# Performance work log

Measured on AMD Instinct MI355X. Metric: run time of the kernel, lower is better.

## Reference

```python
import jax, jax.numpy as jnp
import numpy as np
from jax import lax

F8 = jnp.float8_e4m3fn


def setup_inputs() -> dict:
    key = jax.random.key(0)
    kx, kw = jax.random.split(key)
    x = jax.random.normal(kx, (2, 128, 4, 192, 320), dtype=jnp.float32)
    # matches reset_parameters: normal(0, 0.02) then cast to fp8
    weight = jax.random.normal(kw, (128, 128, 3, 3, 3), dtype=jnp.float32) * 0.02
    return {"x": x, "weight": weight}


def reference(x, weight):
    # fp8 e4m3 quantization round-trip (the torch module stores/consumes fp8),
    # compute/accumulate in fp32 as an fp8 conv kernel would.
    xq = x.astype(F8).astype(jnp.float32)
    wq = weight.astype(F8).astype(jnp.float32)
    # causal temporal padding: (kT-1, 0) = (2, 0); spatial 'same' padding (1,1)
    xp = jnp.pad(xq, ((0, 0), (0, 0), (2, 0), (1, 1), (1, 1)))
    out = lax.conv_general_dilated(
        xp, wq,
        window_strides=(1, 1, 1),
        padding='VALID',
        dimension_numbers=('NCDHW', 'OIDHW', 'NCDHW'),
    )  # (B, 128, 4, 192, 320)
    return out
```

## Files before the change

kernel.cpp:

```cpp
#include <hip/hip_runtime.h>
#include <hip/hip_fp8.h>


using f32x16 = __attribute__((ext_vector_type(16))) float;
using i32x8 = __attribute__((ext_vector_type(8))) int;
typedef long long i64;
struct alignas(16) L2v { i64 x, y; };

namespace {
constexpr int Cc = 128, Dd = 4, Hh = 192, Ww = 320;
constexpr int HP = 194, WP = 322;
constexpr int NTAP = 27;
constexpr size_t PLANE = (size_t)4 * WP * 32;
constexpr size_t XQ_BYTES = (size_t)2 * Dd * HP * PLANE;
constexpr int ZA = 8 * 2 * 2576;
constexpr int ZB = 8 * 192 * 32;
constexpr int GSTR = WP * 32;
constexpr int HB = 1056;
}

__global__ __launch_bounds__(256) void zero_pad_kernel(unsigned char* __restrict__ xq) {
  int i = blockIdx.x * 256 + threadIdx.x;
  if (i < ZA) {
    int bd = i / (2 * 2576);
    int r = i - bd * (2 * 2576);
    int hsel = r / 2576, seg = r - hsel * 2576;
    L2v z{0, 0};
    *(L2v*)(xq + ((size_t)bd * HP + (hsel ? 193 : 0)) * PLANE + (size_t)seg * 16) = z;
  } else if (i < ZA + ZB) {
    int j = i - ZA;
    int bd = j / (192 * 32);
    int r = j - bd * (192 * 32);
    int h = r / 32 + 1;
    int t = r & 31;
    int g = t >> 3, s2 = t & 7;
    int wsel = s2 >> 2, part = s2 & 3;
    *(i64*)(xq + ((size_t)bd * HP + h) * PLANE + (size_t)g * GSTR
            + (size_t)(wsel ? 321 : 0) * 32 + part * 8) = 0;
  }
}

__global__ __launch_bounds__(256) void qx_kernel(const float* __restrict__ x,
                                                 unsigned char* __restrict__ xq) {
  __shared__ unsigned char lt[64 * 136];
  const int tid = threadIdx.x;
  const int b = blockIdx.z >> 2, d = blockIdx.z & 3;
  const int h = blockIdx.y;
  const int w0 = blockIdx.x * 64;
  const int wl = tid & 63, cig = tid >> 6;
  const size_t cstr = (size_t)Dd * Hh * Ww;
  const float* xp = x + (((size_t)b * Cc * Dd + d) * Hh + h) * Ww + w0 + wl;
  #pragma unroll 4
  for (int i = 0; i < 32; ++i) {
    int ci = cig * 32 + i;
    __hip_fp8_e4m3 q(xp[ci * cstr]);
    lt[wl * 136 + ci] = q.__x;
  }
  __syncthreads();
  unsigned char* plane = xq + ((size_t)(b * Dd + d) * HP + h + 1) * PLANE;
  {
    int g = tid >> 6, w = tid & 63;
    const unsigned char* src = lt + w * 136 + g * 32;
    i64 a0 = *(const i64*)(src), a1 = *(const i64*)(src + 8);
    i64 a2 = *(const i64*)(src + 16), a3 = *(const i64*)(src + 24);
    unsigned char* dst = plane + (size_t)g * GSTR + (size_t)(w0 + 1 + w) * 32;
    *(L2v*)dst = L2v{a0, a1};
    *(L2v*)(dst + 16) = L2v{a2, a3};
  }
}

__global__ void wpack_kernel(const float* __restrict__ w, unsigned char* __restrict__ wpk) {
  int idx = blockIdx.x * 256 + threadIdx.x;
  if (idx >= Cc * Cc * NTAP) return;
  int tap = idx % NTAP;
  int t = idx / NTAP;
  int ci = t % Cc, co = t / Cc;
  int cc = ci >> 6, cq = co >> 5;
  int lane = (((ci >> 5) & 1) << 5) | (co & 31);
  __hip_fp8_e4m3 q(w[idx]);
  wpk[((((size_t)tap * 2 + cc) * 4 + cq) * 64 + lane) * 32 + (ci & 31)] = q.__x;
}

__global__ __launch_bounds__(256, 4) void conv_mfma(const unsigned char* __restrict__ xq,
                                                    const unsigned char* __restrict__ wpk,
                                                    float* __restrict__ out) {
  __shared__ unsigned char lb[4 * 4 * 2 * HB];
  const int tid = threadIdx.x;
  const int lane = tid & 63, wv = tid >> 6;
  const int l31 = lane & 31, chalf = lane >> 5;
  const int hr = wv >> 1, ch = wv & 1;
  const int id = blockIdx.x;
  const int xcd = id & 7, j = id >> 3;
  const int h0l = j / 40, rem = j - h0l * 40;
  const int z = rem / 5, wx = rem - z * 5;
  const int b = z >> 2, dout = z & 3;
  const int h0 = (xcd * 12 + h0l) * 2;
  const int w0 = wx * 64;
  const int kdmin = dout >= 2 ? 0 : 2 - dout;

  const unsigned char* bb[3];
  #pragma unroll
  for (int kw = 0; kw < 3; ++kw)
    bb[kw] = lb + (hr * 4 + chalf) * 2 * HB + (l31 + kw) * 16;

  f32x16 acc[2][2];
  #pragma unroll
  for (int a = 0; a < 2; ++a)
    #pragma unroll
    for (int n = 0; n < 2; ++n)
      #pragma unroll
      for (int r = 0; r < 16; ++r) acc[a][n][r] = 0.f;

  for (int kd = kdmin; kd < 3; ++kd) {
    __syncthreads();
    for (int u = tid; u < 1056; u += 256) {
      int w = u % 66, rest = u / 66;
      int g = rest & 3, hrow = rest >> 2;
      const unsigned char* src = xq
          + ((size_t)(b * Dd + dout + kd - 2) * HP + h0 + hrow) * PLANE
          + (size_t)g * GSTR + (size_t)(w0 + w) * 32;
      L2v lo = *(const L2v*)src;
      L2v hi = *(const L2v*)(src + 16);
      unsigned char* base = lb + (hrow * 4 + g) * 2 * HB + w * 16;
      *(L2v*)(base) = lo;
      *(L2v*)(base + HB) = hi;
    }
    __syncthreads();
    __builtin_amdgcn_s_setprio(1);
    #pragma unroll
    for (int kh = 0; kh < 3; ++kh)
      #pragma unroll
      for (int cc = 0; cc < 2; ++cc)
        #pragma unroll
        for (int kw = 0; kw < 3; ++kw) {
          i32x8 av[2];
          #pragma unroll
          for (int ct = 0; ct < 2; ++ct) {
            const unsigned char* ap = wpk +
                ((((size_t)((kd * 9 + kh * 3 + kw) * 2) + cc) * 4 + ch * 2 + ct) * 64 + lane) * 32;
            int4 alo = *(const int4*)ap;
            int4 ahi = *(const int4*)(ap + 16);
            av[ct][0] = alo.x; av[ct][1] = alo.y; av[ct][2] = alo.z; av[ct][3] = alo.w;
            av[ct][4] = ahi.x; av[ct][5] = ahi.y; av[ct][6] = ahi.z; av[ct][7] = ahi.w;
          }
          #pragma unroll
          for (int nf = 0; nf < 2; ++nf) {
            const int off = (kh * 4 + cc * 2) * 2 * HB + nf * 32 * 16;
            int4 blo = *(const int4*)(bb[kw] + off);
            int4 bhi = *(const int4*)(bb[kw] + off + HB);
            i32x8 bv;
            bv[0] = blo.x; bv[1] = blo.y; bv[2] = blo.z; bv[3] = blo.w;
            bv[4] = bhi.x; bv[5] = bhi.y; bv[6] = bhi.z; bv[7] = bhi.w;
            #pragma unroll
            for (int ct = 0; ct < 2; ++ct)
              acc[ct][nf] = __builtin_amdgcn_mfma_scale_f32_32x32x64_f8f6f4(
                  av[ct], bv, acc[ct][nf], 0, 0, 0, 127, 0, 127);
          }
        }
    __builtin_amdgcn_s_setprio(0);
  }

  #pragma unroll
  for (int ct = 0; ct < 2; ++ct)
    #pragma unroll
    for (int nf = 0; nf < 2; ++nf) {
      int ww = w0 + nf * 32 + l31;
      #pragma unroll
      for (int reg = 0; reg < 16; ++reg) {
        int co = ch * 64 + ct * 32 + (reg & 3) + 8 * (reg >> 2) + 4 * chalf;
        out[(((size_t)b * Cc + co) * Dd + dout) * (size_t)(Hh * Ww)
            + (size_t)(h0 + hr) * Ww + ww] = acc[ct][nf][reg];
      }
    }
}

extern "C" void kernel_launch(void* const* d_in, const int* in_sizes, int n_in,
                              void* d_out, int out_size, void* d_ws, size_t ws_size,
                              hipStream_t stream) {
  const float* x = (const float*)d_in[0];
  const float* w = (const float*)d_in[1];
  unsigned char* xq = (unsigned char*)d_ws;
  unsigned char* wpk = xq + XQ_BYTES;
  float* out = (float*)d_out;

  int nz = ZA + ZB;
  zero_pad_kernel<<<(nz + 255) / 256, 256, 0, stream>>>(xq);

  dim3 g1(Ww / 64, Hh, 2 * Dd);
  qx_kernel<<<g1, 256, 0, stream>>>(x, xq);

  int nw = Cc * Cc * NTAP;
  wpack_kernel<<<(nw + 255) / 256, 256, 0, stream>>>(w, wpk);

  conv_mfma<<<dim3(3840), 256, 0, stream>>>(xq, wpk, out);
}
```

Before: 235.4 us.

## Process both batch elements per block to reuse weight fragments across batches

```diff
diff --git a/kernel.cpp b/kernel.cpp
--- a/kernel.cpp
+++ b/kernel.cpp
@@ -4,6 +4,7 @@
 
 using f32x16 = __attribute__((ext_vector_type(16))) float;
 using i32x8 = __attribute__((ext_vector_type(8))) int;
+using i32x4 = __attribute__((ext_vector_type(4))) int;
 typedef long long i64;
 struct alignas(16) L2v { i64 x, y; };
 
@@ -17,6 +18,7 @@
 constexpr int ZB = 8 * 192 * 32;
 constexpr int GSTR = WP * 32;
 constexpr int HB = 1056;
+constexpr int BSTR = 4 * 4 * 2 * HB;
 }
 
 __global__ __launch_bounds__(256) void zero_pad_kernel(unsigned char* __restrict__ xq) {
@@ -81,19 +83,18 @@
   wpk[((((size_t)tap * 2 + cc) * 4 + cq) * 64 + lane) * 32 + (ci & 31)] = q.__x;
 }
 
-__global__ __launch_bounds__(256, 4) void conv_mfma(const unsigned char* __restrict__ xq,
+__global__ __launch_bounds__(256, 2) void conv_mfma(const unsigned char* __restrict__ xq,
                                                     const unsigned char* __restrict__ wpk,
                                                     float* __restrict__ out) {
-  __shared__ unsigned char lb[4 * 4 * 2 * HB];
+  __shared__ unsigned char lb[2 * BSTR];
   const int tid = threadIdx.x;
   const int lane = tid & 63, wv = tid >> 6;
   const int l31 = lane & 31, chalf = lane >> 5;
   const int hr = wv >> 1, ch = wv & 1;
   const int id = blockIdx.x;
   const int xcd = id & 7, j = id >> 3;
-  const int h0l = j / 40, rem = j - h0l * 40;
-  const int z = rem / 5, wx = rem - z * 5;
-  const int b = z >> 2, dout = z & 3;
+  const int h0l = j / 20, rem = j - h0l * 20;
+  const int wx = rem >> 2, dout = rem & 3;
   const int h0 = (xcd * 12 + h0l) * 2;
   const int w0 = wx * 64;
   const int kdmin = dout >= 2 ? 0 : 2 - dout;
@@ -103,25 +104,28 @@
   for (int kw = 0; kw < 3; ++kw)
     bb[kw] = lb + (hr * 4 + chalf) * 2 * HB + (l31 + kw) * 16;
 
-  f32x16 acc[2][2];
+  f32x16 acc[2][2][2];
   #pragma unroll
-  for (int a = 0; a < 2; ++a)
+  for (int s = 0; s < 2; ++s)
     #pragma unroll
-    for (int n = 0; n < 2; ++n)
+    for (int a = 0; a < 2; ++a)
       #pragma unroll
-      for (int r = 0; r < 16; ++r) acc[a][n][r] = 0.f;
+      for (int n = 0; n < 2; ++n)
+        #pragma unroll
+        for (int r = 0; r < 16; ++r) acc[s][a][n][r] = 0.f;
 
   for (int kd = kdmin; kd < 3; ++kd) {
     __syncthreads();
-    for (int u = tid; u < 1056; u += 256) {
+    for (int u = tid; u < 2112; u += 256) {
       int w = u % 66, rest = u / 66;
-      int g = rest & 3, hrow = rest >> 2;
+      int bsel = rest >> 4, r = rest & 15;
+      int g = r & 3, hrow = r >> 2;
       const unsigned char* src = xq
-          + ((size_t)(b * Dd + dout + kd - 2) * HP + h0 + hrow) * PLANE
+          + ((size_t)(bsel * Dd + dout + kd - 2) * HP + h0 + hrow) * PLANE
           + (size_t)g * GSTR + (size_t)(w0 + w) * 32;
       L2v lo = *(const L2v*)src;
       L2v hi = *(const L2v*)(src + 16);
-      unsigned char* base = lb + (hrow * 4 + g) * 2 * HB + w * 16;
+      unsigned char* base = lb + bsel * BSTR + (hrow * 4 + g) * 2 * HB + w * 16;
       *(L2v*)(base) = lo;
       *(L2v*)(base + HB) = hi;
     }
@@ -135,43 +139,40 @@
         for (int kw = 0; kw < 3; ++kw) {
           i32x8 av[2];
           #pragma unroll
-          for (int ct = 0; ct < 2; ++ct) {
-            const unsigned char* ap = wpk +
-                ((((size_t)((kd * 9 + kh * 3 + kw) * 2) + cc) * 4 + ch * 2 + ct) * 64 + lane) * 32;
-            int4 alo = *(const int4*)ap;
-            int4 ahi = *(const int4*)(ap + 16);
-            av[ct][0] = alo.x; av[ct][1] = alo.y; av[ct][2] = alo.z; av[ct][3] = alo.w;
-            av[ct][4] = ahi.x; av[ct][5] = ahi.y; av[ct][6] = ahi.z; av[ct][7] = ahi.w;
-          }
+          for (int ct = 0; ct < 2; ++ct)
+            av[ct] = *(const i32x8*)(wpk +
+                ((((size_t)((kd * 9 + kh * 3 + kw) * 2) + cc) * 4 + ch * 2 + ct) * 64 + lane) * 32);
           #pragma unroll
-          for (int nf = 0; nf < 2; ++nf) {
-            const int off = (kh * 4 + cc * 2) * 2 * HB + nf * 32 * 16;
-            int4 blo = *(const int4*)(bb[kw] + off);
-            int4 bhi = *(const int4*)(bb[kw] + off + HB);
-            i32x8 bv;
-            bv[0] = blo.x; bv[1] = blo.y; bv[2] = blo.z; bv[3] = blo.w;
-            bv[4] = bhi.x; bv[5] = bhi.y; bv[6] = bhi.z; bv[7] = bhi.w;
+          for (int bsel = 0; bsel < 2; ++bsel)
             #pragma unroll
-            for (int ct = 0; ct < 2; ++ct)
-              acc[ct][nf] = __builtin_amdgcn_mfma_scale_f32_32x32x64_f8f6f4(
-                  av[ct], bv, acc[ct][nf], 0, 0, 0, 127, 0, 127);
-          }
+            for (int nf = 0; nf < 2; ++nf) {
+              const int off = bsel * BSTR + (kh * 4 + cc * 2) * 2 * HB + nf * 512;
+              i32x4 blo = *(const i32x4*)(bb[kw] + off);
+              i32x4 bhi = *(const i32x4*)(bb[kw] + off + HB);
+              i32x8 bv = __builtin_shufflevector(blo, bhi, 0, 1, 2, 3, 4, 5, 6, 7);
+              #pragma unroll
+              for (int ct = 0; ct < 2; ++ct)
+                acc[bsel][ct][nf] = __builtin_amdgcn_mfma_scale_f32_32x32x64_f8f6f4(
+                    av[ct], bv, acc[bsel][ct][nf], 0, 0, 0, 127, 0, 127);
+            }
         }
     __builtin_amdgcn_s_setprio(0);
   }
 
   #pragma unroll
-  for (int ct = 0; ct < 2; ++ct)
+  for (int bsel = 0; bsel < 2; ++bsel)
     #pragma unroll
-    for (int nf = 0; nf < 2; ++nf) {
-      int ww = w0 + nf * 32 + l31;
+    for (int ct = 0; ct < 2; ++ct)
       #pragma unroll
-      for (int reg = 0; reg < 16; ++reg) {
-        int co = ch * 64 + ct * 32 + (reg & 3) + 8 * (reg >> 2) + 4 * chalf;
-        out[(((size_t)b * Cc + co) * Dd + dout) * (size_t)(Hh * Ww)
-            + (size_t)(h0 + hr) * Ww + ww] = acc[ct][nf][reg];
+      for (int nf = 0; nf < 2; ++nf) {
+        int ww = w0 + nf * 32 + l31;
+        #pragma unroll
+        for (int reg = 0; reg < 16; ++reg) {
+          int co = ch * 64 + ct * 32 + (reg & 3) + 8 * (reg >> 2) + 4 * chalf;
+          out[(((size_t)bsel * Cc + co) * Dd + dout) * (size_t)(Hh * Ww)
+              + (size_t)(h0 + hr) * Ww + ww] = acc[bsel][ct][nf][reg];
+        }
       }
-    }
 }
 
 extern "C" void kernel_launch(void* const* d_in, const int* in_sizes, int n_in,
@@ -192,5 +193,5 @@
   int nw = Cc * Cc * NTAP;
   wpack_kernel<<<(nw + 255) / 256, 256, 0, stream>>>(w, wpk);
 
-  conv_mfma<<<dim3(3840), 256, 0, stream>>>(xq, wpk, out);
+  conv_mfma<<<dim3(1920), 256, 0, stream>>>(xq, wpk, out);
 }
```

Measured after the change: 259.2 us. +10.1%, slower.

## Double-buffer input slabs in LDS via async global_load_lds prefetch

Applied to the files above, without the earlier changes.

```diff
diff --git a/kernel.cpp b/kernel.cpp
--- a/kernel.cpp
+++ b/kernel.cpp
@@ -4,6 +4,7 @@
 
 using f32x16 = __attribute__((ext_vector_type(16))) float;
 using i32x8 = __attribute__((ext_vector_type(8))) int;
+using i32x4 = __attribute__((ext_vector_type(4))) int;
 typedef long long i64;
 struct alignas(16) L2v { i64 x, y; };
 
@@ -17,6 +18,7 @@
 constexpr int ZB = 8 * 192 * 32;
 constexpr int GSTR = WP * 32;
 constexpr int HB = 1056;
+constexpr int BUFB = 2112 * 16;
 }
 
 __global__ __launch_bounds__(256) void zero_pad_kernel(unsigned char* __restrict__ xq) {
@@ -81,10 +83,21 @@
   wpk[((((size_t)tap * 2 + cc) * 4 + cq) * 64 + lane) * 32 + (ci & 31)] = q.__x;
 }
 
+__device__ __forceinline__ void gll16(const unsigned char* g, unsigned char* l) {
+  __builtin_amdgcn_global_load_lds(
+      (const __attribute__((address_space(1))) void*)g,
+      (__attribute__((address_space(3))) void*)l, 16, 0, 0);
+}
+__device__ __forceinline__ void gll4(const unsigned char* g, unsigned char* l) {
+  __builtin_amdgcn_global_load_lds(
+      (const __attribute__((address_space(1))) void*)g,
+      (__attribute__((address_space(3))) void*)l, 4, 0, 0);
+}
+
 __global__ __launch_bounds__(256, 4) void conv_mfma(const unsigned char* __restrict__ xq,
                                                     const unsigned char* __restrict__ wpk,
                                                     float* __restrict__ out) {
-  __shared__ unsigned char lb[4 * 4 * 2 * HB];
+  __shared__ unsigned char lb[2 * BUFB];
   const int tid = threadIdx.x;
   const int lane = tid & 63, wv = tid >> 6;
   const int l31 = lane & 31, chalf = lane >> 5;
@@ -98,10 +111,30 @@
   const int w0 = wx * 64;
   const int kdmin = dout >= 2 ? 0 : 2 - dout;
 
-  const unsigned char* bb[3];
+  size_t off16[8];
+  int lds16[8];
   #pragma unroll
-  for (int kw = 0; kw < 3; ++kw)
-    bb[kw] = lb + (hr * 4 + chalf) * 2 * HB + (l31 + kw) * 16;
+  for (int it = 0; it < 8; ++it) {
+    int u = it * 256 + tid;
+    int rh = u / 66, w = u - rh * 66;
+    int half = rh & 1, rg = rh >> 1;
+    int g = rg & 3, hrow = rg >> 2;
+    off16[it] = (size_t)(h0 + hrow) * PLANE + (size_t)g * GSTR
+                + (size_t)(w0 + w) * 32 + half * 16;
+    lds16[it] = u * 16;
+  }
+  size_t off4;
+  int lds4 = 32768 + tid * 4;
+  {
+    int q = 2048 + (tid >> 2);
+    int rh = q / 66, w = q - rh * 66;
+    int half = rh & 1, rg = rh >> 1;
+    int g = rg & 3, hrow = rg >> 2;
+    off4 = (size_t)(h0 + hrow) * PLANE + (size_t)g * GSTR
+           + (size_t)(w0 + w) * 32 + half * 16 + (tid & 3) * 4;
+  }
+  const size_t img0 = (size_t)(b * Dd + dout - 2) * HP * PLANE;
+  const size_t imgstep = (size_t)HP * PLANE;
 
   f32x16 acc[2][2];
   #pragma unroll
@@ -111,21 +144,34 @@
       #pragma unroll
       for (int r = 0; r < 16; ++r) acc[a][n][r] = 0.f;
 
+  {
+    const unsigned char* img = xq + img0 + (size_t)kdmin * imgstep;
+    #pragma unroll
+    for (int it = 0; it < 8; ++it) gll16(img + off16[it], lb + lds16[it]);
+    gll4(img + off4, lb + lds4);
+  }
+
+  int p = 0;
   for (int kd = kdmin; kd < 3; ++kd) {
-    __syncthreads();
-    for (int u = tid; u < 1056; u += 256) {
-      int w = u % 66, rest = u / 66;
-      int g = rest & 3, hrow = rest >> 2;
-      const unsigned char* src = xq
-          + ((size_t)(b * Dd + dout + kd - 2) * HP + h0 + hrow) * PLANE
-          + (size_t)g * GSTR + (size_t)(w0 + w) * 32;
-      L2v lo = *(const L2v*)src;
-      L2v hi = *(const L2v*)(src + 16);
-      unsigned char* base = lb + (hrow * 4 + g) * 2 * HB + w * 16;
-      *(L2v*)(base) = lo;
-      *(L2v*)(base + HB) = hi;
+    if (kd + 1 < 3) {
+      const unsigned char* img = xq + img0 + (size_t)(kd + 1) * imgstep;
+      unsigned char* bufn = lb + (p ? 0 : BUFB);
+      #pragma unroll
+      for (int it = 0; it < 8; ++it) gll16(img + off16[it], bufn + lds16[it]);
+      gll4(img + off4, bufn + lds4);
+      asm volatile("s_waitcnt vmcnt(9)" ::: "memory");
+    } else {
+      asm volatile("s_waitcnt vmcnt(0)" ::: "memory");
     }
-    __syncthreads();
+    __builtin_amdgcn_s_barrier();
+    __builtin_amdgcn_sched_barrier(0);
+
+    const unsigned char* bufp = lb + (p ? BUFB : 0);
+    const unsigned char* bb[3];
+    #pragma unroll
+    for (int kw = 0; kw < 3; ++kw)
+      bb[kw] = bufp + (hr * 4 + chalf) * 2 * HB + (l31 + kw) * 16;
+
     __builtin_amdgcn_s_setprio(1);
     #pragma unroll
     for (int kh = 0; kh < 3; ++kh)
@@ -135,22 +181,15 @@
         for (int kw = 0; kw < 3; ++kw) {
           i32x8 av[2];
           #pragma unroll
-          for (int ct = 0; ct < 2; ++ct) {
-            const unsigned char* ap = wpk +
-                ((((size_t)((kd * 9 + kh * 3 + kw) * 2) + cc) * 4 + ch * 2 + ct) * 64 + lane) * 32;
-            int4 alo = *(const int4*)ap;
-            int4 ahi = *(const int4*)(ap + 16);
-            av[ct][0] = alo.x; av[ct][1] = alo.y; av[ct][2] = alo.z; av[ct][3] = alo.w;
-            av[ct][4] = ahi.x; av[ct][5] = ahi.y; av[ct][6] = ahi.z; av[ct][7] = ahi.w;
-          }
+          for (int ct = 0; ct < 2; ++ct)
+            av[ct] = *(const i32x8*)(wpk +
+                ((((size_t)((kd * 9 + kh * 3 + kw) * 2) + cc) * 4 + ch * 2 + ct) * 64 + lane) * 32);
           #pragma unroll
           for (int nf = 0; nf < 2; ++nf) {
-            const int off = (kh * 4 + cc * 2) * 2 * HB + nf * 32 * 16;
-            int4 blo = *(const int4*)(bb[kw] + off);
-            int4 bhi = *(const int4*)(bb[kw] + off + HB);
-            i32x8 bv;
-            bv[0] = blo.x; bv[1] = blo.y; bv[2] = blo.z; bv[3] = blo.w;
-            bv[4] = bhi.x; bv[5] = bhi.y; bv[6] = bhi.z; bv[7] = bhi.w;
+            const int off = (kh * 4 + cc * 2) * 2 * HB + nf * 512;
+            i32x4 blo = *(const i32x4*)(bb[kw] + off);
+            i32x4 bhi = *(const i32x4*)(bb[kw] + off + HB);
+            i32x8 bv = __builtin_shufflevector(blo, bhi, 0, 1, 2, 3, 4, 5, 6, 7);
             #pragma unroll
             for (int ct = 0; ct < 2; ++ct)
               acc[ct][nf] = __builtin_amdgcn_mfma_scale_f32_32x32x64_f8f6f4(
@@ -158,6 +197,8 @@
           }
         }
     __builtin_amdgcn_s_setprio(0);
+    __builtin_amdgcn_s_barrier();
+    p ^= 1;
   }
 
   #pragma unroll
```

Measured after the change: 228.8 us. 2.8% less time.

## Merge prep kernels and software-pipeline weight loads in the MFMA conv loop

Applied to the files above, without the earlier changes.

```diff
diff --git a/kernel.cpp b/kernel.cpp
--- a/kernel.cpp
+++ b/kernel.cpp
@@ -4,6 +4,7 @@
 
 using f32x16 = __attribute__((ext_vector_type(16))) float;
 using i32x8 = __attribute__((ext_vector_type(8))) int;
+using i32x4 = __attribute__((ext_vector_type(4))) int;
 typedef long long i64;
 struct alignas(16) L2v { i64 x, y; };
 
@@ -17,71 +18,77 @@
 constexpr int ZB = 8 * 192 * 32;
 constexpr int GSTR = WP * 32;
 constexpr int HB = 1056;
-}
-
-__global__ __launch_bounds__(256) void zero_pad_kernel(unsigned char* __restrict__ xq) {
-  int i = blockIdx.x * 256 + threadIdx.x;
-  if (i < ZA) {
-    int bd = i / (2 * 2576);
-    int r = i - bd * (2 * 2576);
-    int hsel = r / 2576, seg = r - hsel * 2576;
-    L2v z{0, 0};
-    *(L2v*)(xq + ((size_t)bd * HP + (hsel ? 193 : 0)) * PLANE + (size_t)seg * 16) = z;
-  } else if (i < ZA + ZB) {
-    int j = i - ZA;
-    int bd = j / (192 * 32);
-    int r = j - bd * (192 * 32);
-    int h = r / 32 + 1;
-    int t = r & 31;
-    int g = t >> 3, s2 = t & 7;
-    int wsel = s2 >> 2, part = s2 & 3;
-    *(i64*)(xq + ((size_t)bd * HP + h) * PLANE + (size_t)g * GSTR
-            + (size_t)(wsel ? 321 : 0) * 32 + part * 8) = 0;
-  }
-}
-
-__global__ __launch_bounds__(256) void qx_kernel(const float* __restrict__ x,
-                                                 unsigned char* __restrict__ xq) {
-  __shared__ unsigned char lt[64 * 136];
+constexpr int KDSTR = 9 * 2 * 4 * 64 * 32;
+constexpr int NQX = 5 * 192 * 8;
+constexpr int NZP = (ZA + ZB + 255) / 256;
+constexpr int NWP = (Cc * Cc * NTAP + 255) / 256;
+}
+
+__global__ __launch_bounds__(256) void prep_kernel(const float* __restrict__ x,
+                                                   const float* __restrict__ w,
+                                                   unsigned char* __restrict__ xq,
+                                                   unsigned char* __restrict__ wpk) {
+  const int id = blockIdx.x;
   const int tid = threadIdx.x;
-  const int b = blockIdx.z >> 2, d = blockIdx.z & 3;
-  const int h = blockIdx.y;
-  const int w0 = blockIdx.x * 64;
-  const int wl = tid & 63, cig = tid >> 6;
-  const size_t cstr = (size_t)Dd * Hh * Ww;
-  const float* xp = x + (((size_t)b * Cc * Dd + d) * Hh + h) * Ww + w0 + wl;
-  #pragma unroll 4
-  for (int i = 0; i < 32; ++i) {
-    int ci = cig * 32 + i;
-    __hip_fp8_e4m3 q(xp[ci * cstr]);
-    lt[wl * 136 + ci] = q.__x;
-  }
-  __syncthreads();
-  unsigned char* plane = xq + ((size_t)(b * Dd + d) * HP + h + 1) * PLANE;
-  {
-    int g = tid >> 6, w = tid & 63;
-    const unsigned char* src = lt + w * 136 + g * 32;
+  if (id < NQX) {
+    __shared__ unsigned char lt[64 * 136];
+    const int wx = id % 5;
+    const int h = (id / 5) % 192;
+    const int bd = id / 960;
+    const int b = bd >> 2, d = bd & 3;
+    const int w0 = wx * 64;
+    const int wl = tid & 63, cig = tid >> 6;
+    const size_t cstr = (size_t)Dd * Hh * Ww;
+    const float* xp = x + (((size_t)b * Cc * Dd + d) * Hh + h) * Ww + w0 + wl;
+    #pragma unroll 4
+    for (int i = 0; i < 32; ++i) {
+      int ci = cig * 32 + i;
+      __hip_fp8_e4m3 q(xp[ci * cstr]);
+      lt[wl * 136 + ci] = q.__x;
+    }
+    __syncthreads();
+    unsigned char* plane = xq + ((size_t)(b * Dd + d) * HP + h + 1) * PLANE;
+    int g = tid >> 6, ww = tid & 63;
+    const unsigned char* src = lt + ww * 136 + g * 32;
     i64 a0 = *(const i64*)(src), a1 = *(const i64*)(src + 8);
     i64 a2 = *(const i64*)(src + 16), a3 = *(const i64*)(src + 24);
-    unsigned char* dst = plane + (size_t)g * GSTR + (size_t)(w0 + 1 + w) * 32;
+    unsigned char* dst = plane + (size_t)g * GSTR + (size_t)(w0 + 1 + ww) * 32;
     *(L2v*)dst = L2v{a0, a1};
     *(L2v*)(dst + 16) = L2v{a2, a3};
+  } else if (id < NQX + NZP) {
+    int i = (id - NQX) * 256 + tid;
+    if (i < ZA) {
+      int bd = i / (2 * 2576);
+      int r = i - bd * (2 * 2576);
+      int hsel = r / 2576, seg = r - hsel * 2576;
+      L2v z{0, 0};
+      *(L2v*)(xq + ((size_t)bd * HP + (hsel ? 193 : 0)) * PLANE + (size_t)seg * 16) = z;
+    } else if (i < ZA + ZB) {
+      int j = i - ZA;
+      int bd = j / (192 * 32);
+      int r = j - bd * (192 * 32);
+      int h = r / 32 + 1;
+      int t = r & 31;
+      int g = t >> 3, s2 = t & 7;
+      int wsel = s2 >> 2, part = s2 & 3;
+      *(i64*)(xq + ((size_t)bd * HP + h) * PLANE + (size_t)g * GSTR
+              + (size_t)(wsel ? 321 : 0) * 32 + part * 8) = 0;
+    }
+  } else {
+    int idx = (id - NQX - NZP) * 256 + tid;
+    if (idx < Cc * Cc * NTAP) {
+      int tap = idx % NTAP;
+      int t = idx / NTAP;
+      int ci = t % Cc, co = t / Cc;
+      int cc = ci >> 6, cq = co >> 5;
+      int lane = (((ci >> 5) & 1) << 5) | (co & 31);
+      __hip_fp8_e4m3 q(w[idx]);
+      wpk[((((size_t)tap * 2 + cc) * 4 + cq) * 64 + lane) * 32 + (ci & 31)] = q.__x;
+    }
   }
 }
 
-__global__ void wpack_kernel(const float* __restrict__ w, unsigned char* __restrict__ wpk) {
-  int idx = blockIdx.x * 256 + threadIdx.x;
-  if (idx >= Cc * Cc * NTAP) return;
-  int tap = idx % NTAP;
-  int t = idx / NTAP;
-  int ci = t % Cc, co = t / Cc;
-  int cc = ci >> 6, cq = co >> 5;
-  int lane = (((ci >> 5) & 1) << 5) | (co & 31);
-  __hip_fp8_e4m3 q(w[idx]);
-  wpk[((((size_t)tap * 2 + cc) * 4 + cq) * 64 + lane) * 32 + (ci & 31)] = q.__x;
-}
-
-__global__ __launch_bounds__(256, 4) void conv_mfma(const unsigned char* __restrict__ xq,
+__global__ __launch_bounds__(256, 2) void conv_mfma(const unsigned char* __restrict__ xq,
                                                     const unsigned char* __restrict__ wpk,
                                                     float* __restrict__ out) {
   __shared__ unsigned char lb[4 * 4 * 2 * HB];
@@ -98,6 +105,10 @@
   const int w0 = wx * 64;
   const int kdmin = dout >= 2 ? 0 : 2 - dout;
 
+  const long imgstep = (long)HP * PLANE;
+  const long img0 = (long)(b * Dd + dout - 2) * imgstep;
+  const unsigned char* vbase = wpk + ch * 4096 + lane * 32;
+
   const unsigned char* bb[3];
   #pragma unroll
   for (int kw = 0; kw < 3; ++kw)
@@ -111,13 +122,15 @@
       #pragma unroll
       for (int r = 0; r < 16; ++r) acc[a][n][r] = 0.f;
 
+  i32x8 av[3][2];
+
   for (int kd = kdmin; kd < 3; ++kd) {
     __syncthreads();
+    const unsigned char* img = xq + img0 + (long)kd * imgstep;
     for (int u = tid; u < 1056; u += 256) {
       int w = u % 66, rest = u / 66;
       int g = rest & 3, hrow = rest >> 2;
-      const unsigned char* src = xq
-          + ((size_t)(b * Dd + dout + kd - 2) * HP + h0 + hrow) * PLANE
+      const unsigned char* src = img + (size_t)(h0 + hrow) * PLANE
           + (size_t)g * GSTR + (size_t)(w0 + w) * 32;
       L2v lo = *(const L2v*)src;
       L2v hi = *(const L2v*)(src + 16);
@@ -125,38 +138,50 @@
       *(L2v*)(base) = lo;
       *(L2v*)(base + HB) = hi;
     }
-    __syncthreads();
+    const unsigned char* wkd = vbase + (size_t)kd * KDSTR;
+    #pragma unroll
+    for (int t = 0; t < 2; ++t) {
+      const int kh = t / 6, cc = (t / 3) % 2, kw = t % 3;
+      #pragma unroll
+      for (int ct = 0; ct < 2; ++ct)
+        av[t][ct] = *(const i32x8*)(wkd + (kh * 3 + kw) * 16384 + cc * 8192 + ct * 2048);
+    }
+    asm volatile("s_waitcnt lgkmcnt(0)" ::: "memory");
+    __builtin_amdgcn_s_barrier();
+    __builtin_amdgcn_sched_barrier(0);
+
     __builtin_amdgcn_s_setprio(1);
     #pragma unroll
-    for (int kh = 0; kh < 3; ++kh)
-      #pragma unroll
-      for (int cc = 0; cc < 2; ++cc)
+    for (int t = 0; t < 18; ++t) {
+      const int kh = t / 6, cc = (t / 3) % 2, kw = t % 3;
+      if (t < 16) {
+        const int tp = t + 2;
+        const int khp = tp / 6, ccp = (tp / 3) % 2, kwp = tp % 3;
         #pragma unroll
-        for (int kw = 0; kw < 3; ++kw) {
-          i32x8 av[2];
-          #pragma unroll
-          for (int ct = 0; ct < 2; ++ct) {
-            const unsigned char* ap = wpk +
-                ((((size_t)((kd * 9 + kh * 3 + kw) * 2) + cc) * 4 + ch * 2 + ct) * 64 + lane) * 32;
-            int4 alo = *(const int4*)ap;
-            int4 ahi = *(const int4*)(ap + 16);
-            av[ct][0] = alo.x; av[ct][1] = alo.y; av[ct][2] = alo.z; av[ct][3] = alo.w;
-            av[ct][4] = ahi.x; av[ct][5] = ahi.y; av[ct][6] = ahi.z; av[ct][7] = ahi.w;
-          }
-          #pragma unroll
-          for (int nf = 0; nf < 2; ++nf) {
-            const int off = (kh * 4 + cc * 2) * 2 * HB + nf * 32 * 16;
-            int4 blo = *(const int4*)(bb[kw] + off);
-            int4 bhi = *(const int4*)(bb[kw] + off + HB);
-            i32x8 bv;
-            bv[0] = blo.x; bv[1] = blo.y; bv[2] = blo.z; bv[3] = blo.w;
-            bv[4] = bhi.x; bv[5] = bhi.y; bv[6] = bhi.z; bv[7] = bhi.w;
-            #pragma unroll
-            for (int ct = 0; ct < 2; ++ct)
-              acc[ct][nf] = __builtin_amdgcn_mfma_scale_f32_32x32x64_f8f6f4(
-                  av[ct], bv, acc[ct][nf], 0, 0, 0, 127, 0, 127);
-          }
-        }
+        for (int ct = 0; ct < 2; ++ct)
+          av[tp % 3][ct] =
+              *(const i32x8*)(wkd + (khp * 3 + kwp) * 16384 + ccp * 8192 + ct * 2048);
+      }
+      i32x8 bv[2];
+      #pragma unroll
+      for (int nf = 0; nf < 2; ++nf) {
+        const int off = (kh * 4 + cc * 2) * 2 * HB + nf * 512;
+        i32x4 blo = *(const i32x4*)(bb[kw] + off);
+        i32x4 bhi = *(const i32x4*)(bb[kw] + off + HB);
+        bv[nf] = __builtin_shufflevector(blo, bhi, 0, 1, 2, 3, 4, 5, 6, 7);
+      }
+      if (t < 16)      asm volatile("s_waitcnt vmcnt(4)" ::: "memory");
+      else if (t == 16) asm volatile("s_waitcnt vmcnt(2)" ::: "memory");
+      else              asm volatile("s_waitcnt vmcnt(0)" ::: "memory");
+      asm volatile("s_waitcnt lgkmcnt(0)" ::: "memory");
+      __builtin_amdgcn_sched_barrier(0);
+      #pragma unroll
+      for (int nf = 0; nf < 2; ++nf)
+        #pragma unroll
+        for (int ct = 0; ct < 2; ++ct)
+          acc[ct][nf] = __builtin_amdgcn_mfma_scale_f32_32x32x64_f8f6f4(
+              av[t % 3][ct], bv[nf], acc[ct][nf], 0, 0, 0, 127, 0, 127);
+    }
     __builtin_amdgcn_s_setprio(0);
   }
 
@@ -183,14 +208,6 @@
   unsigned char* wpk = xq + XQ_BYTES;
   float* out = (float*)d_out;
 
-  int nz = ZA + ZB;
-  zero_pad_kernel<<<(nz + 255) / 256, 256, 0, stream>>>(xq);
-
-  dim3 g1(Ww / 64, Hh, 2 * Dd);
-  qx_kernel<<<g1, 256, 0, stream>>>(x, xq);
-
-  int nw = Cc * Cc * NTAP;
-  wpack_kernel<<<(nw + 255) / 256, 256, 0, stream>>>(w, wpk);
-
+  prep_kernel<<<dim3(NQX + NZP + NWP), 256, 0, stream>>>(x, w, xq, wpk);
   conv_mfma<<<dim3(3840), 256, 0, stream>>>(xq, wpk, out);
 }
```

Measured after the change: 222.9 us. 5.3% less time.
